# Kernel tuning notes

Measured on AMD Instinct MI355X. Metric: run time of the kernel, lower is better.

Reference implementation:

```python
import jax, jax.numpy as jnp
import numpy as np

N = 50000
E = 800000
DIMS = [128, 128, 128, 64, 64]  # n_input, hidden[0], hidden[1], hidden[2], n_output


def setup_inputs() -> dict:
    key = jax.random.key(0)
    ks = jax.random.split(key, 16)
    x = jax.random.normal(ks[0], (N, DIMS[0]), dtype=jnp.float32)
    edge_index = jax.random.randint(ks[1], (2, E), 0, N, dtype=jnp.int64)
    inp = {"x": x, "edge_index": edge_index}
    for i in range(4):
        fan_in, fan_out = DIMS[i], DIMS[i + 1]
        scale = 1.0 / jnp.sqrt(jnp.float32(fan_in))
        inp[f"W{i+1}"] = jax.random.normal(ks[2 + 2 * i], (fan_in, fan_out), dtype=jnp.float32) * scale
        inp[f"b{i+1}"] = jnp.zeros((fan_out,), dtype=jnp.float32)
    return inp


def _gcn_norm(edge_index):
    # add self-loops, compute symmetric normalization D^-1/2 (A+I) D^-1/2
    loop = jnp.arange(N, dtype=edge_index.dtype)
    src = jnp.concatenate([edge_index[0], loop])
    dst = jnp.concatenate([edge_index[1], loop])
    ones = jnp.ones(src.shape[0], dtype=jnp.float32)
    deg = jax.ops.segment_sum(ones, dst, num_segments=N)
    dinv = jnp.where(deg > 0, jax.lax.rsqrt(deg), 0.0)
    norm = dinv[src] * dinv[dst]  # [E+N]
    return src, dst, norm


def _gcn_conv(x, W, b, src, dst, norm):
    h = x @ W                                   # [N, out]
    msg = h[src] * norm[:, None]                # gather + scale, [E+N, out]
    agg = jax.ops.segment_sum(msg, dst, num_segments=N)
    return agg + b


def reference(x, edge_index, W1, b1, W2, b2, W3, b3, W4, b4):
    src, dst, norm = _gcn_norm(edge_index)
    h = _gcn_conv(x, W1, b1, src, dst, norm)
    h = jax.nn.selu(h)
    h = _gcn_conv(h, W2, b2, src, dst, norm)
    h = jax.nn.selu(h)
    h = _gcn_conv(h, W3, b3, src, dst, norm)
    h = jax.nn.selu(h)
    h = _gcn_conv(h, W4, b4, src, dst, norm)
    # F.normalize(x): L2 row-normalize with eps=1e-12
    nrm = jnp.sqrt(jnp.sum(h * h, axis=1, keepdims=True))
    return h / jnp.maximum(nrm, 1e-12)
```

## Files before the change

### kernel.cpp

```cpp
#include <hip/hip_runtime.h>
#include <math.h>

#define NN 50000
#define NE 800000
#define NBK ((NN + 255) >> 8)
#define EPB 4096
#define BINA_BLOCKS ((NE + EPB - 1) / EPB)
#define EPT (EPB / 256)

typedef __attribute__((ext_vector_type(8))) __bf16 bf16x8;
typedef __attribute__((ext_vector_type(4))) float f32x4;

__device__ __forceinline__ float selu_f(float x) {
    const float scale = 1.0507009873554805f;
    const float alpha = 1.6732632423543772f;
    return scale * (x > 0.0f ? x : alpha * expm1f(x));
}

__device__ __forceinline__ unsigned rnd_bf16(float f) {
    unsigned u = __float_as_uint(f);
    return (u + 0x7fffu + ((u >> 16) & 1u)) >> 16;
}
__device__ __forceinline__ unsigned pack_pair(float a, float b) {
    return (rnd_bf16(b) << 16) | rnd_bf16(a);
}
__device__ __forceinline__ float lo_f(unsigned u) { return __uint_as_float(u << 16); }
__device__ __forceinline__ float hi_f(unsigned u) { return __uint_as_float(u & 0xffff0000u); }

__global__ void k_hist(const int* __restrict__ dst, int* __restrict__ cnt) {
    int e = blockIdx.x * blockDim.x + threadIdx.x;
    if (e < NE) atomicAdd(&cnt[dst[e]], 1);
}

#define NB1 ((NN + 1023) / 1024)

__global__ void k_scanA(const int* __restrict__ cnt, int* __restrict__ rowptr,
                        int* __restrict__ partials, float* __restrict__ dinv) {
    __shared__ int wsum[4];
    int tid = threadIdx.x;
    int lane = tid & 63, wave = tid >> 6;
    int base = blockIdx.x * 1024 + tid * 4;
    int e0 = 0, e1 = 0, e2 = 0, e3 = 0;
    if (base + 3 < NN) {
        int4 v = *(const int4*)&cnt[base];
        e0 = v.x; e1 = v.y; e2 = v.z; e3 = v.w;
    } else {
        if (base + 0 < NN) e0 = cnt[base + 0];
        if (base + 1 < NN) e1 = cnt[base + 1];
        if (base + 2 < NN) e2 = cnt[base + 2];
        if (base + 3 < NN) e3 = cnt[base + 3];
    }
    if (base + 0 < NN) dinv[base + 0] = rsqrtf((float)(e0 + 1));
    if (base + 1 < NN) dinv[base + 1] = rsqrtf((float)(e1 + 1));
    if (base + 2 < NN) dinv[base + 2] = rsqrtf((float)(e2 + 1));
    if (base + 3 < NN) dinv[base + 3] = rsqrtf((float)(e3 + 1));

    int lsum = e0 + e1 + e2 + e3;
    int s = lsum;
    #pragma unroll
    for (int off = 1; off < 64; off <<= 1) {
        int t = __shfl_up(s, off, 64);
        if (lane >= off) s += t;
    }
    if (lane == 63) wsum[wave] = s;
    __syncthreads();
    int wbase = 0;
    #pragma unroll
    for (int w = 0; w < 4; w++) wbase += (w < wave) ? wsum[w] : 0;
    int excl = wbase + s - lsum;
    if (base + 0 < NN) rowptr[base + 0] = excl;
    if (base + 1 < NN) rowptr[base + 1] = excl + e0;
    if (base + 2 < NN) rowptr[base + 2] = excl + e0 + e1;
    if (base + 3 < NN) rowptr[base + 3] = excl + e0 + e1 + e2;
    if (tid == 0)
        partials[blockIdx.x] = wsum[0] + wsum[1] + wsum[2] + wsum[3];
}

__global__ void k_scanB(int* __restrict__ partials, int* __restrict__ partials2,
                        int* __restrict__ rowptr) {
    int lane = threadIdx.x;
    int v = (lane < NB1) ? partials[lane] : 0;
    int s = v;
    #pragma unroll
    for (int off = 1; off < 64; off <<= 1) {
        int t = __shfl_up(s, off, 64);
        if (lane >= off) s += t;
    }
    if (lane < NB1) partials2[lane] = s - v;
    if (lane == 63) rowptr[NN] = s;
}

__global__ void k_scanC(int* __restrict__ rowptr, const int* __restrict__ partials2,
                        int* __restrict__ bcur) {
    int off = partials2[blockIdx.x];
    int base = blockIdx.x * 1024 + threadIdx.x * 4;
    #pragma unroll
    for (int j = 0; j < 4; j++) {
        int idx = base + j;
        if (idx < NN) {
            int r = rowptr[idx] + off;
            rowptr[idx] = r;
            if ((idx & 255) == 0) bcur[(idx >> 8) * 16] = r;
        }
    }
}

__global__ void __launch_bounds__(256) k_binA(const int* __restrict__ src,
                                              const int* __restrict__ dst,
                                              int* __restrict__ bcur,
                                              int* __restrict__ tmp) {
    __shared__ int hist[NBK];
    __shared__ int gbase[NBK];
    int tid = threadIdx.x;
    for (int i = tid; i < NBK; i += 256) hist[i] = 0;
    __syncthreads();

    const int e0 = blockIdx.x * EPB;
    int rec[EPT];
    int bs[EPT];
    #pragma unroll
    for (int j = 0; j < EPT; j++) {
        int e = e0 + j * 256 + tid;
        if (e < NE) {
            int s = src[e], d = dst[e];
            int b = d >> 8;
            int slot = atomicAdd(&hist[b], 1);
            rec[j] = (s << 8) | (d & 255);
            bs[j] = (b << 16) | slot;
        } else {
            bs[j] = -1;
        }
    }
    __syncthreads();
    for (int i = tid; i < NBK; i += 256)
        gbase[i] = atomicAdd(&bcur[i * 16], hist[i]);
    __syncthreads();
    #pragma unroll
    for (int j = 0; j < EPT; j++) {
        if (bs[j] >= 0) {
            int b = bs[j] >> 16, slot = bs[j] & 0xffff;
            tmp[gbase[b] + slot] = rec[j];
        }
    }
}

__global__ void __launch_bounds__(256) k_binB(const int* __restrict__ tmp,
                                              const int* __restrict__ rowptr,
                                              const float* __restrict__ dinv,
                                              int2* __restrict__ edat) {
    __shared__ int lpos[256];
    __shared__ float ldin[256];
    int b = blockIdx.x, tid = threadIdx.x;
    int n0 = b << 8;
    int n = n0 + tid;
    if (n < NN) { lpos[tid] = rowptr[n]; ldin[tid] = dinv[n]; }
    int base = rowptr[n0];
    int end  = rowptr[(n0 + 256 < NN) ? n0 + 256 : NN];
    __syncthreads();
    for (int i = base + tid; i < end; i += 256) {
        int rc = tmp[i];
        int s = rc >> 8;
        int dl = rc & 255;
        float nm = dinv[s] * ldin[dl];
        int slot = atomicAdd(&lpos[dl], 1);
        edat[slot] = make_int2(s, __float_as_int(nm));
    }
}

__global__ void k_packx(const float* __restrict__ x, unsigned* __restrict__ tabX) {
    long u = (long)blockIdx.x * 256 + threadIdx.x;
    if (u * 4 < (long)NN * 64) {
        const float4* ip = (const float4*)&x[u * 8];
        float4 a = ip[0], b = ip[1];
        uint4 o;
        o.x = pack_pair(a.x, a.y); o.y = pack_pair(a.z, a.w);
        o.z = pack_pair(b.x, b.y); o.w = pack_pair(b.z, b.w);
        *(uint4*)&tabX[u * 4] = o;
    }
}

template <int K, int J>
__global__ void __launch_bounds__(256) k_mm4(const unsigned* __restrict__ tabin,
                                             const float* __restrict__ W,
                                             unsigned* __restrict__ out) {
    constexpr int K2 = K / 2;
    constexpr int STRIDE = K2 + 4;
    constexpr int CT = J / 16;
    constexpr int KC = K / 32;
    constexpr int J2 = J / 2;

    __shared__ unsigned Wt[J * STRIDE];

    for (int u = threadIdx.x; u < J * K2; u += 256) {
        int col = u % J, kk = u / J;
        Wt[col * STRIDE + kk] = pack_pair(W[(2 * kk) * J + col], W[(2 * kk + 1) * J + col]);
    }
    __syncthreads();

    const int w = threadIdx.x >> 6, l = threadIdx.x & 63;
    const int lr = l & 15, lk = l >> 4;
    const long r0 = (long)blockIdx.x * 128 + w * 32;

    f32x4 acc[CT][2];
    #pragma unroll
    for (int t = 0; t < CT; t++) {
        acc[t][0] = (f32x4)(0.0f);
        acc[t][1] = (f32x4)(0.0f);
    }

    #pragma unroll
    for (int kc = 0; kc < KC; kc++) {
        uint4 a0u = *(const uint4*)&tabin[(r0 + lr) * K2 + kc * 16 + lk * 4];
        uint4 a1u = *(const uint4*)&tabin[(r0 + 16 + lr) * K2 + kc * 16 + lk * 4];
        bf16x8 a0 = __builtin_bit_cast(bf16x8, a0u);
        bf16x8 a1 = __builtin_bit_cast(bf16x8, a1u);
        #pragma unroll
        for (int t = 0; t < CT; t++) {
            uint4 bu = *(const uint4*)&Wt[(t * 16 + lr) * STRIDE + kc * 16 + lk * 4];
            bf16x8 b = __builtin_bit_cast(bf16x8, bu);
            acc[t][0] = __builtin_amdgcn_mfma_f32_16x16x32_bf16(a0, b, acc[t][0], 0, 0, 0);
            acc[t][1] = __builtin_amdgcn_mfma_f32_16x16x32_bf16(a1, b, acc[t][1], 0, 0, 0);
        }
    }

    #pragma unroll
    for (int t = 0; t < CT; t++) {
        #pragma unroll
        for (int s = 0; s < 2; s++) {
            f32x4 d = acc[t][s];
            #pragma unroll
            for (int i = 0; i < 4; i++) {
                float v = d[i];
                float vp = __shfl_xor(v, 1);
                long row = r0 + s * 16 + lk * 4 + i;
                if (!(l & 1) && row < NN)
                    out[row * J2 + t * 8 + (lr >> 1)] = pack_pair(v, vp);
            }
        }
    }
}

template <bool DO_SELU, bool PACK>
__global__ void k_agg128(const unsigned* __restrict__ tab, const int* __restrict__ rowptr,
                         const int2* __restrict__ edat, const float* __restrict__ dinv,
                         const float* __restrict__ bias, void* __restrict__ out_) {
    int n = (blockIdx.x * blockDim.x + threadIdx.x) >> 6;
    int lane = threadIdx.x & 63;
    if (n >= NN) return;
    float dn = dinv[n];
    float self = dn * dn;
    int beg = rowptr[n], end = rowptr[n + 1];

    float2 bv = ((const float2*)bias)[lane];
    unsigned su = tab[(size_t)n * 64 + lane];
    float ax = bv.x + self * lo_f(su);
    float ay = bv.y + self * hi_f(su);

    int e = beg;
    for (; e + 7 < end; e += 8) {
        int2 m0 = edat[e + 0], m1 = edat[e + 1], m2 = edat[e + 2], m3 = edat[e + 3];
        int2 m4 = edat[e + 4], m5 = edat[e + 5], m6 = edat[e + 6], m7 = edat[e + 7];
        unsigned g0 = tab[(size_t)m0.x * 64 + lane];
        unsigned g1 = tab[(size_t)m1.x * 64 + lane];
        unsigned g2 = tab[(size_t)m2.x * 64 + lane];
        unsigned g3 = tab[(size_t)m3.x * 64 + lane];
        unsigned g4 = tab[(size_t)m4.x * 64 + lane];
        unsigned g5 = tab[(size_t)m5.x * 64 + lane];
        unsigned g6 = tab[(size_t)m6.x * 64 + lane];
        unsigned g7 = tab[(size_t)m7.x * 64 + lane];
        float w0 = __int_as_float(m0.y), w1 = __int_as_float(m1.y);
        float w2 = __int_as_float(m2.y), w3 = __int_as_float(m3.y);
        float w4 = __int_as_float(m4.y), w5 = __int_as_float(m5.y);
        float w6 = __int_as_float(m6.y), w7 = __int_as_float(m7.y);
        ax += w0 * lo_f(g0); ay += w0 * hi_f(g0);
        ax += w1 * lo_f(g1); ay += w1 * hi_f(g1);
        ax += w2 * lo_f(g2); ay += w2 * hi_f(g2);
        ax += w3 * lo_f(g3); ay += w3 * hi_f(g3);
        ax += w4 * lo_f(g4); ay += w4 * hi_f(g4);
        ax += w5 * lo_f(g5); ay += w5 * hi_f(g5);
        ax += w6 * lo_f(g6); ay += w6 * hi_f(g6);
        ax += w7 * lo_f(g7); ay += w7 * hi_f(g7);
    }
    for (; e < end; e++) {
        int2 m = edat[e];
        float w = __int_as_float(m.y);
        unsigned g = tab[(size_t)m.x * 64 + lane];
        ax += w * lo_f(g); ay += w * hi_f(g);
    }
    if constexpr (DO_SELU) { ax = selu_f(ax); ay = selu_f(ay); }
    if constexpr (PACK)
        ((unsigned*)out_)[(size_t)n * 64 + lane] = pack_pair(ax, ay);
    else
        ((float2*)out_)[(size_t)n * 64 + lane] = make_float2(ax, ay);
}

template <bool DO_SELU, bool DO_NORM, bool PACK>
__global__ void k_agg64(const unsigned* __restrict__ tab, const int* __restrict__ rowptr,
                        const int2* __restrict__ edat, const float* __restrict__ dinv,
                        const float* __restrict__ bias, void* __restrict__ out_) {
    int n = (blockIdx.x * blockDim.x + threadIdx.x) >> 6;
    int lane = threadIdx.x & 63;
    if (n >= NN) return;
    int half = lane >> 5;
    int sub = lane & 31;
    float dn = dinv[n];
    float self = dn * dn;
    int beg = rowptr[n], end = rowptr[n + 1];

    float a0 = 0.f, a1 = 0.f;
    int e = beg + half;
    for (; e + 6 < end; e += 8) {
        int2 m0 = edat[e + 0], m1 = edat[e + 2], m2 = edat[e + 4], m3 = edat[e + 6];
        unsigned g0 = tab[(size_t)m0.x * 32 + sub];
        unsigned g1 = tab[(size_t)m1.x * 32 + sub];
        unsigned g2 = tab[(size_t)m2.x * 32 + sub];
        unsigned g3 = tab[(size_t)m3.x * 32 + sub];
        float w0 = __int_as_float(m0.y), w1 = __int_as_float(m1.y);
        float w2 = __int_as_float(m2.y), w3 = __int_as_float(m3.y);
        a0 += w0 * lo_f(g0); a1 += w0 * hi_f(g0);
        a0 += w1 * lo_f(g1); a1 += w1 * hi_f(g1);
        a0 += w2 * lo_f(g2); a1 += w2 * hi_f(g2);
        a0 += w3 * lo_f(g3); a1 += w3 * hi_f(g3);
    }
    for (; e < end; e += 2) {
        int2 m = edat[e];
        float w = __int_as_float(m.y);
        unsigned g = tab[(size_t)m.x * 32 + sub];
        a0 += w * lo_f(g); a1 += w * hi_f(g);
    }
    a0 += __shfl_xor(a0, 32);
    a1 += __shfl_xor(a1, 32);
    float2 bv = ((const float2*)bias)[sub];
    unsigned su = tab[(size_t)n * 32 + sub];
    a0 += bv.x + self * lo_f(su);
    a1 += bv.y + self * hi_f(su);
    if constexpr (DO_SELU) { a0 = selu_f(a0); a1 = selu_f(a1); }
    if constexpr (DO_NORM) {
        float ss = a0 * a0 + a1 * a1;
        #pragma unroll
        for (int off = 16; off > 0; off >>= 1) ss += __shfl_xor(ss, off);
        float nrm = sqrtf(ss);
        float inv = 1.0f / fmaxf(nrm, 1e-12f);
        a0 *= inv; a1 *= inv;
    }
    if (half == 0) {
        if constexpr (PACK)
            ((unsigned*)out_)[(size_t)n * 32 + sub] = pack_pair(a0, a1);
        else
            ((float2*)out_)[(size_t)n * 32 + sub] = make_float2(a0, a1);
    }
}

extern "C" void kernel_launch(void* const* d_in, const int* in_sizes, int n_in,
                              void* d_out, int out_size, void* d_ws, size_t ws_size,
                              hipStream_t stream) {
    const float* x  = (const float*)d_in[0];
    const int* edge = (const int*)d_in[1];
    const float* W1 = (const float*)d_in[2]; const float* b1 = (const float*)d_in[3];
    const float* W2 = (const float*)d_in[4]; const float* b2 = (const float*)d_in[5];
    const float* W3 = (const float*)d_in[6]; const float* b3 = (const float*)d_in[7];
    const float* W4 = (const float*)d_in[8]; const float* b4 = (const float*)d_in[9];
    float* out = (float*)d_out;

    char* ws = (char*)d_ws;
    size_t off = 0;
    auto alloc = [&](size_t bytes) -> void* {
        void* p = ws + off;
        off = (off + bytes + 255) & ~(size_t)255;
        return p;
    };
    int*      cnt    = (int*)alloc((size_t)NN * 4);
    int*      rowptr = (int*)alloc((size_t)(NN + 1) * 4);
    float*    dinv   = (float*)alloc((size_t)NN * 4);
    int*      tmp    = (int*)alloc((size_t)NE * 4);
    int2*     edat   = (int2*)alloc((size_t)NE * 8);
    unsigned* tabX   = (unsigned*)alloc((size_t)(NN + 128) * 64 * 4);
    unsigned* tab    = (unsigned*)alloc((size_t)(NN + 128) * 64 * 4);
    unsigned* bufU   = (unsigned*)alloc((size_t)(NN + 128) * 64 * 4);
    int*      part1  = (int*)alloc(64 * 4);
    int*      part2  = (int*)alloc(64 * 4);
    int*      bcur   = (int*)alloc((size_t)NBK * 16 * 4);

    const int* srcp = edge;
    const int* dstp = edge + NE;

    const int BE = (NE + 255) / 256;

    hipMemsetAsync(cnt, 0, (size_t)NN * 4, stream);
    k_hist<<<BE, 256, 0, stream>>>(dstp, cnt);
    k_scanA<<<NB1, 256, 0, stream>>>(cnt, rowptr, part1, dinv);
    k_scanB<<<1, 64, 0, stream>>>(part1, part2, rowptr);
    k_scanC<<<NB1, 256, 0, stream>>>(rowptr, part2, bcur);
    k_binA<<<BINA_BLOCKS, 256, 0, stream>>>(srcp, dstp, bcur, tmp);
    k_binB<<<NBK, 256, 0, stream>>>(tmp, rowptr, dinv, edat);

    const int AGG_B = (NN + 3) / 4;
    const int MMB = (NN + 127) / 128;
    const int PXB = ((NN * 64 / 4) + 255) / 256;

    k_packx<<<PXB, 256, 0, stream>>>(x, tabX);

    k_mm4<128, 128><<<MMB, 256, 0, stream>>>(tabX, W1, tab);
    k_agg128<true, true><<<AGG_B, 256, 0, stream>>>(tab, rowptr, edat, dinv, b1, bufU);
    k_mm4<128, 128><<<MMB, 256, 0, stream>>>(bufU, W2, tab);
    k_agg128<true, true><<<AGG_B, 256, 0, stream>>>(tab, rowptr, edat, dinv, b2, bufU);
    k_mm4<128, 64><<<MMB, 256, 0, stream>>>(bufU, W3, tab);
    k_agg64<true, false, true><<<AGG_B, 256, 0, stream>>>(tab, rowptr, edat, dinv, b3, bufU);
    k_mm4<64, 64><<<MMB, 256, 0, stream>>>(bufU, W4, tab);
    k_agg64<false, true, false><<<AGG_B, 256, 0, stream>>>(tab, rowptr, edat, dinv, b4, out);
}
```

Baseline: 354.0 us.

## Widen aggregation gathers to 16-byte loads and prepack weights once

The aggregation kernels now split each wavefront into edge groups (4 groups of 16 lanes for 128-wide, 8 groups of 8 lanes for 64-wide). Each lane gathers a uint4 of 8 bf16 features per edge, and the partial sums are reduced across groups with shuffles. This raises bytes per load instruction and the number of edges in flight, in exchange for more registers and a cross-lane reduction at the end. Separately, a new kernel converts all four weight matrices to packed bf16 once, so the matmul kernels copy them into shared memory with vector loads instead of repacking fp32 weights in every block.

```diff
diff --git a/kernel.cpp b/kernel.cpp
--- a/kernel.cpp
+++ b/kernel.cpp
@@ -179,9 +179,24 @@
     }
 }
 
+__global__ void k_packw(const float* __restrict__ W1, const float* __restrict__ W2,
+                        const float* __restrict__ W3, const float* __restrict__ W4,
+                        unsigned* __restrict__ Wp) {
+    int u = blockIdx.x * 256 + threadIdx.x;
+    const float* W; int J, K2, off;
+    if (u < 8192)       { W = W1; J = 128; K2 = 64; off = 0; }
+    else if (u < 16384) { W = W2; J = 128; K2 = 64; off = 8192; }
+    else if (u < 20480) { W = W3; J = 64;  K2 = 64; off = 16384; }
+    else if (u < 22528) { W = W4; J = 64;  K2 = 32; off = 20480; }
+    else return;
+    int v = u - off;
+    int col = v / K2, kk = v % K2;
+    Wp[u] = pack_pair(W[(2 * kk) * J + col], W[(2 * kk + 1) * J + col]);
+}
+
 template <int K, int J>
 __global__ void __launch_bounds__(256) k_mm4(const unsigned* __restrict__ tabin,
-                                             const float* __restrict__ W,
+                                             const unsigned* __restrict__ Wp,
                                              unsigned* __restrict__ out) {
     constexpr int K2 = K / 2;
     constexpr int STRIDE = K2 + 4;
@@ -191,9 +206,10 @@
 
     __shared__ unsigned Wt[J * STRIDE];
 
-    for (int u = threadIdx.x; u < J * K2; u += 256) {
-        int col = u % J, kk = u / J;
-        Wt[col * STRIDE + kk] = pack_pair(W[(2 * kk) * J + col], W[(2 * kk + 1) * J + col]);
+    for (int u4 = threadIdx.x; u4 < J * K2 / 4; u4 += 256) {
+        int v = u4 * 4;
+        int col = v / K2, kk = v % K2;
+        *(uint4*)&Wt[col * STRIDE + kk] = *(const uint4*)&Wp[v];
     }
     __syncthreads();
 
@@ -240,114 +256,143 @@
     }
 }
 
-template <bool DO_SELU, bool PACK>
-__global__ void k_agg128(const unsigned* __restrict__ tab, const int* __restrict__ rowptr,
+template <bool DO_SELU>
+__global__ void k_agg128w(const unsigned* __restrict__ tab, const int* __restrict__ rowptr,
+                          const int2* __restrict__ edat, const float* __restrict__ dinv,
+                          const float* __restrict__ bias, unsigned* __restrict__ outp) {
+    int n = (blockIdx.x * blockDim.x + threadIdx.x) >> 6;
+    int l = threadIdx.x & 63;
+    if (n >= NN) return;
+    int g = l >> 4, sub = l & 15;
+    int beg = rowptr[n], end = rowptr[n + 1];
+
+    float ax[8] = {0.f, 0.f, 0.f, 0.f, 0.f, 0.f, 0.f, 0.f};
+    int e = beg + g;
+    for (; e + 4 < end; e += 8) {
+        int2 m0 = edat[e], m1 = edat[e + 4];
+        uint4 v0 = *(const uint4*)&tab[(size_t)m0.x * 64 + sub * 4];
+        uint4 v1 = *(const uint4*)&tab[(size_t)m1.x * 64 + sub * 4];
+        float w0 = __int_as_float(m0.y), w1 = __int_as_float(m1.y);
+        ax[0] += w0 * lo_f(v0.x); ax[1] += w0 * hi_f(v0.x);
+        ax[2] += w0 * lo_f(v0.y); ax[3] += w0 * hi_f(v0.y);
+        ax[4] += w0 * lo_f(v0.z); ax[5] += w0 * hi_f(v0.z);
+        ax[6] += w0 * lo_f(v0.w); ax[7] += w0 * hi_f(v0.w);
+        ax[0] += w1 * lo_f(v1.x); ax[1] += w1 * hi_f(v1.x);
+        ax[2] += w1 * lo_f(v1.y); ax[3] += w1 * hi_f(v1.y);
+        ax[4] += w1 * lo_f(v1.z); ax[5] += w1 * hi_f(v1.z);
+        ax[6] += w1 * lo_f(v1.w); ax[7] += w1 * hi_f(v1.w);
+    }
+    for (; e < end; e += 4) {
+        int2 m = edat[e];
+        uint4 v = *(const uint4*)&tab[(size_t)m.x * 64 + sub * 4];
+        float w = __int_as_float(m.y);
+        ax[0] += w * lo_f(v.x); ax[1] += w * hi_f(v.x);
+        ax[2] += w * lo_f(v.y); ax[3] += w * hi_f(v.y);
+        ax[4] += w * lo_f(v.z); ax[5] += w * hi_f(v.z);
+        ax[6] += w * lo_f(v.w); ax[7] += w * hi_f(v.w);
+    }
+    #pragma unroll
+    for (int d = 0; d < 8; d++) {
+        ax[d] += __shfl_xor(ax[d], 16);
+        ax[d] += __shfl_xor(ax[d], 32);
+    }
+    if (g == 0) {
+        float dn = dinv[n];
+        float self = dn * dn;
+        uint4 su = *(const uint4*)&tab[(size_t)n * 64 + sub * 4];
+        float4 b0 = *(const float4*)&bias[sub * 8];
+        float4 b1 = *(const float4*)&bias[sub * 8 + 4];
+        ax[0] += b0.x + self * lo_f(su.x); ax[1] += b0.y + self * hi_f(su.x);
+        ax[2] += b0.z + self * lo_f(su.y); ax[3] += b0.w + self * hi_f(su.y);
+        ax[4] += b1.x + self * lo_f(su.z); ax[5] += b1.y + self * hi_f(su.z);
+        ax[6] += b1.z + self * lo_f(su.w); ax[7] += b1.w + self * hi_f(su.w);
+        if constexpr (DO_SELU) {
+            #pragma unroll
+            for (int d = 0; d < 8; d++) ax[d] = selu_f(ax[d]);
+        }
+        uint4 o;
+        o.x = pack_pair(ax[0], ax[1]); o.y = pack_pair(ax[2], ax[3]);
+        o.z = pack_pair(ax[4], ax[5]); o.w = pack_pair(ax[6], ax[7]);
+        *(uint4*)&outp[(size_t)n * 64 + sub * 4] = o;
+    }
+}
+
+template <bool DO_SELU, bool DO_NORM, bool PACK>
+__global__ void k_agg64w(const unsigned* __restrict__ tab, const int* __restrict__ rowptr,
                          const int2* __restrict__ edat, const float* __restrict__ dinv,
                          const float* __restrict__ bias, void* __restrict__ out_) {
     int n = (blockIdx.x * blockDim.x + threadIdx.x) >> 6;
-    int lane = threadIdx.x & 63;
+    int l = threadIdx.x & 63;
     if (n >= NN) return;
-    float dn = dinv[n];
-    float self = dn * dn;
+    int g = l >> 3, sub = l & 7;
     int beg = rowptr[n], end = rowptr[n + 1];
 
-    float2 bv = ((const float2*)bias)[lane];
-    unsigned su = tab[(size_t)n * 64 + lane];
-    float ax = bv.x + self * lo_f(su);
-    float ay = bv.y + self * hi_f(su);
-
-    int e = beg;
-    for (; e + 7 < end; e += 8) {
-        int2 m0 = edat[e + 0], m1 = edat[e + 1], m2 = edat[e + 2], m3 = edat[e + 3];
-        int2 m4 = edat[e + 4], m5 = edat[e + 5], m6 = edat[e + 6], m7 = edat[e + 7];
-        unsigned g0 = tab[(size_t)m0.x * 64 + lane];
-        unsigned g1 = tab[(size_t)m1.x * 64 + lane];
-        unsigned g2 = tab[(size_t)m2.x * 64 + lane];
-        unsigned g3 = tab[(size_t)m3.x * 64 + lane];
-        unsigned g4 = tab[(size_t)m4.x * 64 + lane];
-        unsigned g5 = tab[(size_t)m5.x * 64 + lane];
-        unsigned g6 = tab[(size_t)m6.x * 64 + lane];
-        unsigned g7 = tab[(size_t)m7.x * 64 + lane];
+    float ax[8] = {0.f, 0.f, 0.f, 0.f, 0.f, 0.f, 0.f, 0.f};
+    int e = beg + g;
+    for (; e + 8 < end; e += 16) {
+        int2 m0 = edat[e], m1 = edat[e + 8];
+        uint4 v0 = *(const uint4*)&tab[(size_t)m0.x * 32 + sub * 4];
+        uint4 v1 = *(const uint4*)&tab[(size_t)m1.x * 32 + sub * 4];
         float w0 = __int_as_float(m0.y), w1 = __int_as_float(m1.y);
-        float w2 = __int_as_float(m2.y), w3 = __int_as_float(m3.y);
-        float w4 = __int_as_float(m4.y), w5 = __int_as_float(m5.y);
-        float w6 = __int_as_float(m6.y), w7 = __int_as_float(m7.y);
-        ax += w0 * lo_f(g0); ay += w0 * hi_f(g0);
-        ax += w1 * lo_f(g1); ay += w1 * hi_f(g1);
-        ax += w2 * lo_f(g2); ay += w2 * hi_f(g2);
-        ax += w3 * lo_f(g3); ay += w3 * hi_f(g3);
-        ax += w4 * lo_f(g4); ay += w4 * hi_f(g4);
-        ax += w5 * lo_f(g5); ay += w5 * hi_f(g5);
-        ax += w6 * lo_f(g6); ay += w6 * hi_f(g6);
-        ax += w7 * lo_f(g7); ay += w7 * hi_f(g7);
-    }
-    for (; e < end; e++) {
+        ax[0] += w0 * lo_f(v0.x); ax[1] += w0 * hi_f(v0.x);
+        ax[2] += w0 * lo_f(v0.y); ax[3] += w0 * hi_f(v0.y);
+        ax[4] += w0 * lo_f(v0.z); ax[5] += w0 * hi_f(v0.z);
+        ax[6] += w0 * lo_f(v0.w); ax[7] += w0 * hi_f(v0.w);
+        ax[0] += w1 * lo_f(v1.x); ax[1] += w1 * hi_f(v1.x);
+        ax[2] += w1 * lo_f(v1.y); ax[3] += w1 * hi_f(v1.y);
+        ax[4] += w1 * lo_f(v1.z); ax[5] += w1 * hi_f(v1.z);
+        ax[6] += w1 * lo_f(v1.w); ax[7] += w1 * hi_f(v1.w);
+    }
+    for (; e < end; e += 8) {
         int2 m = edat[e];
+        uint4 v = *(const uint4*)&tab[(size_t)m.x * 32 + sub * 4];
         float w = __int_as_float(m.y);
-        unsigned g = tab[(size_t)m.x * 64 + lane];
-        ax += w * lo_f(g); ay += w * hi_f(g);
-    }
-    if constexpr (DO_SELU) { ax = selu_f(ax); ay = selu_f(ay); }
-    if constexpr (PACK)
-        ((unsigned*)out_)[(size_t)n * 64 + lane] = pack_pair(ax, ay);
-    else
-        ((float2*)out_)[(size_t)n * 64 + lane] = make_float2(ax, ay);
-}
-
-template <bool DO_SELU, bool DO_NORM, bool PACK>
-__global__ void k_agg64(const unsigned* __restrict__ tab, const int* __restrict__ rowptr,
-                        const int2* __restrict__ edat, const float* __restrict__ dinv,
-                        const float* __restrict__ bias, void* __restrict__ out_) {
-    int n = (blockIdx.x * blockDim.x + threadIdx.x) >> 6;
-    int lane = threadIdx.x & 63;
-    if (n >= NN) return;
-    int half = lane >> 5;
-    int sub = lane & 31;
-    float dn = dinv[n];
-    float self = dn * dn;
-    int beg = rowptr[n], end = rowptr[n + 1];
-
-    float a0 = 0.f, a1 = 0.f;
-    int e = beg + half;
-    for (; e + 6 < end; e += 8) {
-        int2 m0 = edat[e + 0], m1 = edat[e + 2], m2 = edat[e + 4], m3 = edat[e + 6];
-        unsigned g0 = tab[(size_t)m0.x * 32 + sub];
-        unsigned g1 = tab[(size_t)m1.x * 32 + sub];
-        unsigned g2 = tab[(size_t)m2.x * 32 + sub];
-        unsigned g3 = tab[(size_t)m3.x * 32 + sub];
-        float w0 = __int_as_float(m0.y), w1 = __int_as_float(m1.y);
-        float w2 = __int_as_float(m2.y), w3 = __int_as_float(m3.y);
-        a0 += w0 * lo_f(g0); a1 += w0 * hi_f(g0);
-        a0 += w1 * lo_f(g1); a1 += w1 * hi_f(g1);
-        a0 += w2 * lo_f(g2); a1 += w2 * hi_f(g2);
-        a0 += w3 * lo_f(g3); a1 += w3 * hi_f(g3);
-    }
-    for (; e < end; e += 2) {
-        int2 m = edat[e];
-        float w = __int_as_float(m.y);
-        unsigned g = tab[(size_t)m.x * 32 + sub];
-        a0 += w * lo_f(g); a1 += w * hi_f(g);
-    }
-    a0 += __shfl_xor(a0, 32);
-    a1 += __shfl_xor(a1, 32);
-    float2 bv = ((const float2*)bias)[sub];
-    unsigned su = tab[(size_t)n * 32 + sub];
-    a0 += bv.x + self * lo_f(su);
-    a1 += bv.y + self * hi_f(su);
-    if constexpr (DO_SELU) { a0 = selu_f(a0); a1 = selu_f(a1); }
-    if constexpr (DO_NORM) {
-        float ss = a0 * a0 + a1 * a1;
-        #pragma unroll
-        for (int off = 16; off > 0; off >>= 1) ss += __shfl_xor(ss, off);
-        float nrm = sqrtf(ss);
-        float inv = 1.0f / fmaxf(nrm, 1e-12f);
-        a0 *= inv; a1 *= inv;
-    }
-    if (half == 0) {
-        if constexpr (PACK)
-            ((unsigned*)out_)[(size_t)n * 32 + sub] = pack_pair(a0, a1);
-        else
-            ((float2*)out_)[(size_t)n * 32 + sub] = make_float2(a0, a1);
+        ax[0] += w * lo_f(v.x); ax[1] += w * hi_f(v.x);
+        ax[2] += w * lo_f(v.y); ax[3] += w * hi_f(v.y);
+        ax[4] += w * lo_f(v.z); ax[5] += w * hi_f(v.z);
+        ax[6] += w * lo_f(v.w); ax[7] += w * hi_f(v.w);
+    }
+    #pragma unroll
+    for (int d = 0; d < 8; d++) {
+        ax[d] += __shfl_xor(ax[d], 8);
+        ax[d] += __shfl_xor(ax[d], 16);
+        ax[d] += __shfl_xor(ax[d], 32);
+    }
+    if (g == 0) {
+        float dn = dinv[n];
+        float self = dn * dn;
+        uint4 su = *(const uint4*)&tab[(size_t)n * 32 + sub * 4];
+        float4 b0 = *(const float4*)&bias[sub * 8];
+        float4 b1 = *(const float4*)&bias[sub * 8 + 4];
+        ax[0] += b0.x + self * lo_f(su.x); ax[1] += b0.y + self * hi_f(su.x);
+        ax[2] += b0.z + self * lo_f(su.y); ax[3] += b0.w + self * hi_f(su.y);
+        ax[4] += b1.x + self * lo_f(su.z); ax[5] += b1.y + self * hi_f(su.z);
+        ax[6] += b1.z + self * lo_f(su.w); ax[7] += b1.w + self * hi_f(su.w);
+        if constexpr (DO_SELU) {
+            #pragma unroll
+            for (int d = 0; d < 8; d++) ax[d] = selu_f(ax[d]);
+        }
+        if constexpr (DO_NORM) {
+            float ss = 0.f;
+            #pragma unroll
+            for (int d = 0; d < 8; d++) ss += ax[d] * ax[d];
+            ss += __shfl_xor(ss, 1);
+            ss += __shfl_xor(ss, 2);
+            ss += __shfl_xor(ss, 4);
+            float inv = 1.0f / fmaxf(sqrtf(ss), 1e-12f);
+            #pragma unroll
+            for (int d = 0; d < 8; d++) ax[d] *= inv;
+        }
+        if constexpr (PACK) {
+            uint4 o;
+            o.x = pack_pair(ax[0], ax[1]); o.y = pack_pair(ax[2], ax[3]);
+            o.z = pack_pair(ax[4], ax[5]); o.w = pack_pair(ax[6], ax[7]);
+            *(uint4*)&((unsigned*)out_)[(size_t)n * 32 + sub * 4] = o;
+        } else {
+            float* op = (float*)out_ + (size_t)n * 64 + sub * 8;
+            *(float4*)op = make_float4(ax[0], ax[1], ax[2], ax[3]);
+            *(float4*)(op + 4) = make_float4(ax[4], ax[5], ax[6], ax[7]);
+        }
     }
 }
 
@@ -377,6 +422,7 @@
     unsigned* tabX   = (unsigned*)alloc((size_t)(NN + 128) * 64 * 4);
     unsigned* tab    = (unsigned*)alloc((size_t)(NN + 128) * 64 * 4);
     unsigned* bufU   = (unsigned*)alloc((size_t)(NN + 128) * 64 * 4);
+    unsigned* Wp     = (unsigned*)alloc((size_t)22528 * 4);
     int*      part1  = (int*)alloc(64 * 4);
     int*      part2  = (int*)alloc(64 * 4);
     int*      bcur   = (int*)alloc((size_t)NBK * 16 * 4);
@@ -398,14 +444,15 @@
     const int MMB = (NN + 127) / 128;
     const int PXB = ((NN * 64 / 4) + 255) / 256;
 
+    k_packw<<<88, 256, 0, stream>>>(W1, W2, W3, W4, Wp);
     k_packx<<<PXB, 256, 0, stream>>>(x, tabX);
 
-    k_mm4<128, 128><<<MMB, 256, 0, stream>>>(tabX, W1, tab);
-    k_agg128<true, true><<<AGG_B, 256, 0, stream>>>(tab, rowptr, edat, dinv, b1, bufU);
-    k_mm4<128, 128><<<MMB, 256, 0, stream>>>(bufU, W2, tab);
-    k_agg128<true, true><<<AGG_B, 256, 0, stream>>>(tab, rowptr, edat, dinv, b2, bufU);
-    k_mm4<128, 64><<<MMB, 256, 0, stream>>>(bufU, W3, tab);
-    k_agg64<true, false, true><<<AGG_B, 256, 0, stream>>>(tab, rowptr, edat, dinv, b3, bufU);
-    k_mm4<64, 64><<<MMB, 256, 0, stream>>>(bufU, W4, tab);
-    k_agg64<false, true, false><<<AGG_B, 256, 0, stream>>>(tab, rowptr, edat, dinv, b4, out);
-}
+    k_mm4<128, 128><<<MMB, 256, 0, stream>>>(tabX, Wp, tab);
+    k_agg128w<true><<<AGG_B, 256, 0, stream>>>(tab, rowptr, edat, dinv, b1, bufU);
+    k_mm4<128, 128><<<MMB, 256, 0, stream>>>(bufU, Wp + 8192, tab);
+    k_agg128w<true><<<AGG_B, 256, 0, stream>>>(tab, rowptr, edat, dinv, b2, bufU);
+    k_mm4<128, 64><<<MMB, 256, 0, stream>>>(bufU, Wp + 16384, tab);
+    k_agg64w<true, false, true><<<AGG_B, 256, 0, stream>>>(tab, rowptr, edat, dinv, b3, bufU);
+    k_mm4<64, 64><<<MMB, 256, 0, stream>>>(bufU, Wp + 20480, tab);
+    k_agg64w<false, true, false><<<AGG_B, 256, 0, stream>>>(tab, rowptr, edat, dinv, b4, out);
+}
```

Result: faster. 336.8 us (-4.9%).
